# Performance work log

Hardware: AMD Instinct MI355X
Metric: run time of the kernel (lower is better)

## Reference

```python
import jax, jax.numpy as jnp
import numpy as np

H = 16  # num_heads

def setup_inputs() -> dict:
    key = jax.random.key(0)
    ks = jax.random.split(key, 9)
    B, S, E = 2, 2048, 1024
    d = E // H  # 64, shared KV head dim
    sc = lambda n: 1.0 / np.sqrt(n)
    return {
        "x": jax.random.normal(ks[0], (B, S, E), jnp.float32),
        "wq": jax.random.normal(ks[1], (E, E), jnp.float32) * sc(E),
        "bq": jax.random.normal(ks[2], (E,), jnp.float32) * 0.02,
        "wk": jax.random.normal(ks[3], (E, d), jnp.float32) * sc(E),
        "bk": jax.random.normal(ks[4], (d,), jnp.float32) * 0.02,
        "wv": jax.random.normal(ks[5], (E, d), jnp.float32) * sc(E),
        "bv": jax.random.normal(ks[6], (d,), jnp.float32) * 0.02,
        "wo": jax.random.normal(ks[7], (E, E), jnp.float32) * sc(E),
        "bo": jax.random.normal(ks[8], (E,), jnp.float32) * 0.02,
    }

def reference(x, wq, bq, wk, bk, wv, bv, wo, bo):
    B, S, E = x.shape
    d = E // H
    Q = (x @ wq + bq).reshape(B, S, H, d).transpose(0, 2, 1, 3)  # [B,H,S,d]
    K = x @ wk + bk  # [B,S,d] shared across heads (MQA)
    V = x @ wv + bv  # [B,S,d]
    scores = jnp.einsum('bhqd,bkd->bhqk', Q, K) / np.sqrt(d)  # [B,H,S,S]
    weights = jax.nn.softmax(scores, axis=-1)
    attn = jnp.einsum('bhqk,bkd->bhqd', weights, V)  # [B,H,S,d]
    # FAITHFUL to source: reshape [B,H,S,d] -> [B,S,E] WITHOUT permuting back
    attn = attn.reshape(B, S, E)
    return attn @ wo + bo
```

## Files before the change

kernel.cpp:

```cpp
#include <hip/hip_runtime.h>
#include <hip/hip_bf16.h>

#define BB 2
#define SS 2048
#define EE 1024
#define HH 16
#define DD 64

using bfrag  = __attribute__((ext_vector_type(8))) short;
using bfrag4 = __attribute__((ext_vector_type(4))) short;
using ffrag  = __attribute__((ext_vector_type(4))) float;
using uint2v = __attribute__((ext_vector_type(2))) uint;
using uint4v = __attribute__((ext_vector_type(4))) uint;

#define MFMA32(A, B, C) __builtin_amdgcn_mfma_f32_16x16x32_bf16(A, B, C, 0, 0, 0)
#define MFMA16(A, B, C) __builtin_amdgcn_mfma_f32_16x16x16bf16_1k(A, B, C, 0, 0, 0)

static __device__ __forceinline__ ushort f2bf(float f) {
  __hip_bfloat16 h = __float2bfloat16(f);
  return *reinterpret_cast<ushort*>(&h);
}

static __device__ __forceinline__ uint pack_bf2(float lo, float hi) {
  uint a = __float_as_uint(lo) + 0x8000u;
  uint b = __float_as_uint(hi) + 0x8000u;
  return __builtin_amdgcn_perm(b, a, 0x07060302u);
}

static __device__ __forceinline__ void gl_lds16(const ushort* g, ushort* l) {
  __builtin_amdgcn_global_load_lds(
      (const __attribute__((address_space(1))) void*)g,
      (__attribute__((address_space(3))) void*)l, 16, 0, 0);
}

__global__ __launch_bounds__(256) void prep(
    const float* __restrict__ x, const float* __restrict__ wq,
    const float* __restrict__ wk, const float* __restrict__ wv,
    const float* __restrict__ wo, ushort* __restrict__ xb,
    ushort* __restrict__ wqkvT, ushort* __restrict__ woT) {
  __shared__ float t[32][33];
  int id = blockIdx.x;
  if (id < 4096) {
    int i = id * 256 + threadIdx.x;
    float4 v = ((const float4*)x)[i];
    ushort4 u = { f2bf(v.x), f2bf(v.y), f2bf(v.z), f2bf(v.w) };
    ((ushort4*)xb)[i] = u;
    return;
  }
  id -= 4096;
  const float* src;
  ushort* dst;
  int N, bx, by;
  if (id < 1024)      { src = wq; dst = wqkvT;                      N = 1024; bx = id & 31;          by = id >> 5; }
  else if (id < 2048) { src = wo; dst = woT;                        N = 1024; bx = (id - 1024) & 31; by = (id - 1024) >> 5; }
  else if (id < 2112) { src = wk; dst = wqkvT + (size_t)1024 * 1024; N = 64;  bx = (id - 2048) & 1;  by = (id - 2048) >> 1; }
  else                { src = wv; dst = wqkvT + (size_t)1088 * 1024; N = 64;  bx = (id - 2112) & 1;  by = (id - 2112) >> 1; }
  const int k0 = by * 32, n0 = bx * 32;
  const int tx = threadIdx.x & 31, ty = threadIdx.x >> 5;
  #pragma unroll
  for (int i = 0; i < 32; i += 8)
    t[ty + i][tx] = src[(size_t)(k0 + ty + i) * N + n0 + tx];
  __syncthreads();
  #pragma unroll
  for (int i = 0; i < 32; i += 8)
    dst[(size_t)(n0 + ty + i) * 1024 + k0 + tx] = f2bf(t[tx][ty + i]);
}

template <bool QKV>
__global__ __launch_bounds__(256) void gemm_mfma3(
    const ushort* __restrict__ A, const ushort* __restrict__ Bt,
    const float* __restrict__ bias0, const float* __restrict__ bias1,
    const float* __restrict__ bias2, void* __restrict__ O1,
    ushort* __restrict__ Kb, ushort* __restrict__ VTb,
    int M, int N, int K, float qscale) {
  __shared__ __align__(16) ushort As[2][128 * 64];
  __shared__ __align__(16) ushort Bs[2][64 * 64];
  const int tid = threadIdx.x;
  const int lane = tid & 63;
  const int quad = lane >> 4;
  const int c = lane & 15;
  const int wv = tid >> 6;
  const int wm = (wv & 1) * 64;
  const int wn = (wv >> 1) * 32;
  const size_t m0 = (size_t)blockIdx.y * 128;
  const size_t n0 = (size_t)blockIdx.x * 64;

  const int srow = lane >> 3;
  const int sck = (lane & 7) ^ srow;

  ffrag zero = {0.f, 0.f, 0.f, 0.f};
  ffrag acc[4][2];
  #pragma unroll
  for (int mt = 0; mt < 4; ++mt)
    #pragma unroll
    for (int nt = 0; nt < 2; ++nt) acc[mt][nt] = zero;

  const int NK = K >> 6;
  #pragma unroll
  for (int i = 0; i < 4; ++i) {
    int ia = wv * 4 + i;
    gl_lds16(&A[(m0 + ia * 8 + srow) * (size_t)K + sck * 8], &As[0][ia * 512]);
  }
  #pragma unroll
  for (int i = 0; i < 2; ++i) {
    int ib = wv * 2 + i;
    gl_lds16(&Bt[(n0 + ib * 8 + srow) * (size_t)K + sck * 8], &Bs[0][ib * 512]);
  }
  __syncthreads();

  for (int ki = 0; ki < NK; ++ki) {
    const int buf = ki & 1;
    if (ki + 1 < NK) {
      int k0 = (ki + 1) << 6;
      #pragma unroll
      for (int i = 0; i < 4; ++i) {
        int ia = wv * 4 + i;
        gl_lds16(&A[(m0 + ia * 8 + srow) * (size_t)K + k0 + sck * 8],
                 &As[buf ^ 1][ia * 512]);
      }
      #pragma unroll
      for (int i = 0; i < 2; ++i) {
        int ib = wv * 2 + i;
        gl_lds16(&Bt[(n0 + ib * 8 + srow) * (size_t)K + k0 + sck * 8],
                 &Bs[buf ^ 1][ib * 512]);
      }
    }
    #pragma unroll
    for (int ks = 0; ks < 2; ++ks) {
      bfrag af[4], bf[2];
      #pragma unroll
      for (int mt = 0; mt < 4; ++mt) {
        int ra = wm + mt * 16 + c;
        af[mt] = *(const bfrag*)&As[buf][(ra * 8 + ((ks * 4 + quad) ^ (ra & 7))) * 8];
      }
      #pragma unroll
      for (int nt = 0; nt < 2; ++nt) {
        int rb = wn + nt * 16 + c;
        bf[nt] = *(const bfrag*)&Bs[buf][(rb * 8 + ((ks * 4 + quad) ^ (rb & 7))) * 8];
      }
      #pragma unroll
      for (int mt = 0; mt < 4; ++mt)
        #pragma unroll
        for (int nt = 0; nt < 2; ++nt)
          acc[mt][nt] = MFMA32(af[mt], bf[nt], acc[mt][nt]);
    }
    __syncthreads();
  }

  #pragma unroll
  for (int nt = 0; nt < 2; ++nt) {
    const int colb = (int)n0 + wn + nt * 16;
    if (QKV) {
      if (colb < 1024) {
        float bb = bias0[colb + c];
        ushort* dst = (ushort*)O1 + colb;
        #pragma unroll
        for (int mt = 0; mt < 4; ++mt)
          #pragma unroll
          for (int r = 0; r < 4; ++r) {
            size_t row = m0 + wm + mt * 16 + quad * 4 + r;
            dst[row * 1024 + c] = f2bf((acc[mt][nt][r] + bb) * qscale);
          }
      } else if (colb < 1088) {
        float bb = bias1[colb - 1024 + c];
        ushort* dst = Kb + (colb - 1024);
        #pragma unroll
        for (int mt = 0; mt < 4; ++mt)
          #pragma unroll
          for (int r = 0; r < 4; ++r) {
            size_t row = m0 + wm + mt * 16 + quad * 4 + r;
            dst[row * 64 + c] = f2bf(acc[mt][nt][r] + bb);
          }
      } else {
        int d = colb - 1088 + c;
        float bb = bias2[colb - 1088 + c];
        int bidx = (int)(m0 >> 11);
        ushort* dstv = VTb + ((size_t)(bidx * 64 + d)) * SS;
        #pragma unroll
        for (int mt = 0; mt < 4; ++mt) {
          int sb = (int)(m0 & 2047) + wm + mt * 16 + quad * 4;
          uint2v u;
          u.x = pack_bf2(acc[mt][nt][0] + bb, acc[mt][nt][1] + bb);
          u.y = pack_bf2(acc[mt][nt][2] + bb, acc[mt][nt][3] + bb);
          *(uint2v*)&dstv[sb] = u;
        }
      }
    } else {
      float bb = bias0[colb + c];
      float* dst = (float*)O1;
      #pragma unroll
      for (int mt = 0; mt < 4; ++mt)
        #pragma unroll
        for (int r = 0; r < 4; ++r) {
          size_t row = m0 + wm + mt * 16 + quad * 4 + r;
          dst[row * (size_t)N + colb + c] = acc[mt][nt][r] + bb;
        }
    }
  }
}

__global__ __launch_bounds__(512) void mqa_attn12(
    const ushort* __restrict__ Q, const ushort* __restrict__ Kg,
    const ushort* __restrict__ VT, ushort* __restrict__ A2) {
  __shared__ __align__(16) ushort Kt[2][2][4096];
  __shared__ __align__(16) ushort Vt[2][2][4096];
  const int tid = threadIdx.x;
  const int lane = tid & 63;
  const int quad = lane >> 4;
  const int c = lane & 15;
  const int wv = tid >> 6;
  const int half = wv >> 2;
  const int lw = wv & 3;
  const int bid = blockIdx.x;
  const int b = bid >> 8;
  const int r = bid & 255;
  const int h = r >> 4;
  const int s0 = (r & 15) << 7;

  const int srow = lane >> 3;
  const int sck = (lane & 7) ^ srow;

  ffrag zero = {0.f, 0.f, 0.f, 0.f};
  bfrag4 ones4;
  #pragma unroll
  for (int i = 0; i < 4; ++i) ones4[i] = (short)16256;

  bfrag aq[2][2];
  #pragma unroll
  for (int mt = 0; mt < 2; ++mt) {
    const ushort* qp =
        Q + ((size_t)(b * SS) + s0 + lw * 32 + mt * 16 + c) * EE + h * 64 + quad * 8;
    aq[mt][0] = *(const bfrag*)qp;
    aq[mt][1] = *(const bfrag*)(qp + 32);
  }

  ffrag o[2][4];
  #pragma unroll
  for (int mt = 0; mt < 2; ++mt)
    #pragma unroll
    for (int nt = 0; nt < 4; ++nt) o[mt][nt] = zero;
  ffrag ls[2] = {zero, zero};

  const int koff = half << 10;
  const ushort* Kbase = Kg + (size_t)b * SS * 64;
  const ushort* Vbase = VT + (size_t)b * 64 * SS;
  const int i0 = lw * 2, i1 = lw * 2 + 1;
  const int r0 = i0 * 8 + srow, r1 = i1 * 8 + srow;

  const int jj = lane & 7;
  const int d0 = lw * 16 + (lane >> 3);
  const int d1 = d0 + 8;
  const ushort* vsrc0 = Vbase + (size_t)d0 * SS + jj * 8;
  const ushort* vsrc1 = Vbase + (size_t)d1 * SS + jj * 8;
  const int q00 = d0 * 64 + (((jj * 2)     ^ (d0 & 15)) * 4);
  const int q01 = d0 * 64 + (((jj * 2 + 1) ^ (d0 & 15)) * 4);
  const int q10 = d1 * 64 + (((jj * 2)     ^ (d1 & 15)) * 4);
  const int q11 = d1 * 64 + (((jj * 2 + 1) ^ (d1 & 15)) * 4);

  {
    uint4v v0 = *(const uint4v*)(vsrc0 + koff);
    uint4v v1 = *(const uint4v*)(vsrc1 + koff);
    gl_lds16(Kbase + (size_t)(koff + r0) * 64 + sck * 8, &Kt[half][0][i0 * 512]);
    gl_lds16(Kbase + (size_t)(koff + r1) * 64 + sck * 8, &Kt[half][0][i1 * 512]);
    ushort* vdst = &Vt[half][0][0];
    *(uint2v*)&vdst[q00] = (uint2v){v0[0], v0[1]};
    *(uint2v*)&vdst[q01] = (uint2v){v0[2], v0[3]};
    *(uint2v*)&vdst[q10] = (uint2v){v1[0], v1[1]};
    *(uint2v*)&vdst[q11] = (uint2v){v1[2], v1[3]};
  }
  __syncthreads();

  for (int it = 0; it < 16; ++it) {
    const int buf = it & 1;
    uint4v nv0, nv1;
    if (it + 1 < 16) {
      int kb = koff + ((it + 1) << 6);
      nv0 = *(const uint4v*)(vsrc0 + kb);
      nv1 = *(const uint4v*)(vsrc1 + kb);
      gl_lds16(Kbase + (size_t)(kb + r0) * 64 + sck * 8, &Kt[half][buf ^ 1][i0 * 512]);
      gl_lds16(Kbase + (size_t)(kb + r1) * 64 + sck * 8, &Kt[half][buf ^ 1][i1 * 512]);
    }

    #pragma unroll
    for (int kt = 0; kt < 4; ++kt) {
      const int key = kt * 16 + c;
      const int k7 = key & 7;
      bfrag kf0 = *(const bfrag*)&Kt[half][buf][(key * 8 + (quad ^ k7)) * 8];
      bfrag kf1 = *(const bfrag*)&Kt[half][buf][(key * 8 + ((quad + 4) ^ k7)) * 8];
      bfrag4 pb[2];
      #pragma unroll
      for (int mt = 0; mt < 2; ++mt) {
        ffrag st = MFMA32(kf0, aq[mt][0], zero);
        st = MFMA32(kf1, aq[mt][1], st);
        uint2v uu;
        uu.x = pack_bf2(__builtin_amdgcn_exp2f(st[0]),
                        __builtin_amdgcn_exp2f(st[1]));
        uu.y = pack_bf2(__builtin_amdgcn_exp2f(st[2]),
                        __builtin_amdgcn_exp2f(st[3]));
        pb[mt] = __builtin_bit_cast(bfrag4, uu);
      }
      const int vg = kt * 4 + quad;
      #pragma unroll
      for (int nt = 0; nt < 4; ++nt) {
        int d = nt * 16 + c;
        bfrag4 vf = *(const bfrag4*)&Vt[half][buf][d * 64 + ((vg ^ c) * 4)];
        #pragma unroll
        for (int mt = 0; mt < 2; ++mt)
          o[mt][nt] = MFMA16(vf, pb[mt], o[mt][nt]);
      }
      #pragma unroll
      for (int mt = 0; mt < 2; ++mt)
        ls[mt] = MFMA16(ones4, pb[mt], ls[mt]);
    }

    if (it + 1 < 16) {
      ushort* vdst = &Vt[half][buf ^ 1][0];
      *(uint2v*)&vdst[q00] = (uint2v){nv0[0], nv0[1]};
      *(uint2v*)&vdst[q01] = (uint2v){nv0[2], nv0[3]};
      *(uint2v*)&vdst[q10] = (uint2v){nv1[0], nv1[1]};
      *(uint2v*)&vdst[q11] = (uint2v){nv1[2], nv1[3]};
    }
    __syncthreads();
  }

  float* cbuf = (float*)&Kt[0][0][0];
  float* lbuf = (float*)&Vt[0][0][0];
  if (half == 1) {
    float* wb = cbuf + (size_t)lw * 2048;
    #pragma unroll
    for (int mt = 0; mt < 2; ++mt) {
      #pragma unroll
      for (int nt = 0; nt < 4; ++nt)
        *(ffrag*)&wb[(mt * 4 + nt) * 256 + lane * 4] = o[mt][nt];
      lbuf[lw * 128 + mt * 64 + lane] = ls[mt][0];
    }
  }
  __syncthreads();
  if (half == 1) return;

  const float* rb = cbuf + (size_t)lw * 2048;
  #pragma unroll
  for (int mt = 0; mt < 2; ++mt) {
    #pragma unroll
    for (int nt = 0; nt < 4; ++nt) {
      ffrag p = *(const ffrag*)&rb[(mt * 4 + nt) * 256 + lane * 4];
      o[mt][nt] += p;
    }
    const float inv = 1.f / (ls[mt][0] + lbuf[lw * 128 + mt * 64 + lane]);
    const int sp = h * 128 + (s0 >> 4) + lw * 2 + mt;
    ushort* orow = A2 + ((size_t)b * SS + sp) * EE;
    #pragma unroll
    for (int nt = 0; nt < 4; ++nt) {
      uint2v u;
      u.x = pack_bf2(o[mt][nt][0] * inv, o[mt][nt][1] * inv);
      u.y = pack_bf2(o[mt][nt][2] * inv, o[mt][nt][3] * inv);
      *(uint2v*)&orow[c * 64 + nt * 16 + quad * 4] = u;
    }
  }
}

extern "C" void kernel_launch(void* const* d_in, const int* in_sizes, int n_in,
                              void* d_out, int out_size, void* d_ws, size_t ws_size,
                              hipStream_t stream) {
  const float* x  = (const float*)d_in[0];
  const float* wq = (const float*)d_in[1];
  const float* bq = (const float*)d_in[2];
  const float* wk = (const float*)d_in[3];
  const float* bk = (const float*)d_in[4];
  const float* wv = (const float*)d_in[5];
  const float* bv = (const float*)d_in[6];
  const float* wo = (const float*)d_in[7];
  const float* bo = (const float*)d_in[8];
  float* out = (float*)d_out;

  char* w = (char*)d_ws;
  ushort* xb     = (ushort*)w;  w += (size_t)4096 * 1024 * 2;
  ushort* wqkvT  = (ushort*)w;  w += (size_t)1152 * 1024 * 2;
  ushort* woT    = (ushort*)w;  w += (size_t)1024 * 1024 * 2;
  ushort* Qb     = (ushort*)w;  w += (size_t)4096 * 1024 * 2;
  ushort* Kb     = (ushort*)w;  w += (size_t)4096 * 64 * 2;
  ushort* VTb    = (ushort*)w;  w += (size_t)BB * 64 * SS * 2;
  ushort* A2     = (ushort*)w;  w += (size_t)4096 * 1024 * 2;

  prep<<<6272, 256, 0, stream>>>(x, wq, wk, wv, wo, xb, wqkvT, woT);

  const float qscale = 0.18033688011112042f;
  gemm_mfma3<true><<<dim3(18, 32), 256, 0, stream>>>(
      xb, wqkvT, bq, bk, bv, Qb, Kb, VTb, 4096, 1152, 1024, qscale);

  mqa_attn12<<<512, 512, 0, stream>>>(Qb, Kb, VTb, A2);

  gemm_mfma3<false><<<dim3(16, 32), 256, 0, stream>>>(
      A2, woT, bo, nullptr, nullptr, out, nullptr, nullptr, 4096, 1024, 1024, 1.0f);
}
```

Before: 171.1 us.

## Triple-buffer GEMM LDS staging with partial vmcnt waits

Moves the projection GEMM from double to triple buffering of its A/B LDS tiles, issuing global-to-LDS loads two k-steps ahead. Each iteration waits with a partial vmcnt count so only the oldest tile's loads must land, and uses a raw s_barrier in place of __syncthreads. The intent is to hide more global load latency behind MFMA work. In exchange, LDS use grows from 48KB to 72KB per block, which can lower occupancy, and correctness now depends on the hand-written vmcnt counts matching the number of loads issued.

```diff
diff --git a/kernel.cpp b/kernel.cpp
--- a/kernel.cpp
+++ b/kernel.cpp
@@ -73,8 +73,8 @@
     const float* __restrict__ bias2, void* __restrict__ O1,
     ushort* __restrict__ Kb, ushort* __restrict__ VTb,
     int M, int N, int K, float qscale) {
-  __shared__ __align__(16) ushort As[2][128 * 64];
-  __shared__ __align__(16) ushort Bs[2][64 * 64];
+  __shared__ __align__(16) ushort As[3][128 * 64];
+  __shared__ __align__(16) ushort Bs[3][64 * 64];
   const int tid = threadIdx.x;
   const int lane = tid & 63;
   const int quad = lane >> 4;
@@ -96,35 +96,38 @@
     for (int nt = 0; nt < 2; ++nt) acc[mt][nt] = zero;
 
   const int NK = K >> 6;
-  #pragma unroll
-  for (int i = 0; i < 4; ++i) {
-    int ia = wv * 4 + i;
-    gl_lds16(&A[(m0 + ia * 8 + srow) * (size_t)K + sck * 8], &As[0][ia * 512]);
-  }
-  #pragma unroll
-  for (int i = 0; i < 2; ++i) {
-    int ib = wv * 2 + i;
-    gl_lds16(&Bt[(n0 + ib * 8 + srow) * (size_t)K + sck * 8], &Bs[0][ib * 512]);
-  }
-  __syncthreads();
+
+  auto stage = [&](int kt, int sb) {
+    const int k0 = kt << 6;
+    #pragma unroll
+    for (int i = 0; i < 4; ++i) {
+      int ia = wv * 4 + i;
+      gl_lds16(&A[(m0 + ia * 8 + srow) * (size_t)K + k0 + sck * 8],
+               &As[sb][ia * 512]);
+    }
+    #pragma unroll
+    for (int i = 0; i < 2; ++i) {
+      int ib = wv * 2 + i;
+      gl_lds16(&Bt[(n0 + ib * 8 + srow) * (size_t)K + k0 + sck * 8],
+               &Bs[sb][ib * 512]);
+    }
+  };
+
+  stage(0, 0);
+  if (NK > 1) {
+    stage(1, 1);
+    asm volatile("s_waitcnt vmcnt(6)" ::: "memory");
+  } else {
+    asm volatile("s_waitcnt vmcnt(0)" ::: "memory");
+  }
+  __builtin_amdgcn_sched_barrier(0);
+  __builtin_amdgcn_s_barrier();
+  __builtin_amdgcn_sched_barrier(0);
 
   for (int ki = 0; ki < NK; ++ki) {
-    const int buf = ki & 1;
-    if (ki + 1 < NK) {
-      int k0 = (ki + 1) << 6;
-      #pragma unroll
-      for (int i = 0; i < 4; ++i) {
-        int ia = wv * 4 + i;
-        gl_lds16(&A[(m0 + ia * 8 + srow) * (size_t)K + k0 + sck * 8],
-                 &As[buf ^ 1][ia * 512]);
-      }
-      #pragma unroll
-      for (int i = 0; i < 2; ++i) {
-        int ib = wv * 2 + i;
-        gl_lds16(&Bt[(n0 + ib * 8 + srow) * (size_t)K + k0 + sck * 8],
-                 &Bs[buf ^ 1][ib * 512]);
-      }
-    }
+    const int buf = ki % 3;
+    if (ki + 2 < NK) stage(ki + 2, (ki + 2) % 3);
+
     #pragma unroll
     for (int ks = 0; ks < 2; ++ks) {
       bfrag af[4], bf[2];
@@ -144,7 +147,14 @@
         for (int nt = 0; nt < 2; ++nt)
           acc[mt][nt] = MFMA32(af[mt], bf[nt], acc[mt][nt]);
     }
-    __syncthreads();
+
+    if (ki + 1 < NK) {
+      if (ki + 2 < NK) asm volatile("s_waitcnt vmcnt(6)" ::: "memory");
+      else             asm volatile("s_waitcnt vmcnt(0)" ::: "memory");
+      __builtin_amdgcn_sched_barrier(0);
+      __builtin_amdgcn_s_barrier();
+      __builtin_amdgcn_sched_barrier(0);
+    }
   }
 
   #pragma unroll
```

Result: slower. 182.6 us (+6.7%).
